# Optimization experiments

Measured on AMD Instinct MI355X. Metric: run time of the kernel, lower is better.

The kernel has to match this reference:

```python
import jax, jax.numpy as jnp
import numpy as np

WINDOW = 512      # sliding window size (causal: keys in [m-WINDOW+1, m])
NEG_INF = -1e30   # large negative instead of -inf for fp16/bf16 safety


def setup_inputs() -> dict:
    key = jax.random.key(0)
    kq, kk, kv = jax.random.split(key, 3)
    B, S, H, Hk, D = 1, 8192, 32, 8, 128
    q = jax.random.normal(kq, (B, S, H, D), dtype=jnp.float32)
    k = jax.random.normal(kk, (B, S, Hk, D), dtype=jnp.float32)
    v = jax.random.normal(kv, (B, S, Hk, D), dtype=jnp.float32)
    return {"q": q, "k": k, "v": v}


def _swa_causal(q, k, v, window):
    """Causal sliding-window attention with GQA, banded (no SxS matrix)."""
    B, S, H, D = q.shape
    Hk = k.shape[2]
    G = H // Hk                      # query heads per kv head
    C = window                        # query block size
    nb = S // C                       # number of query blocks (S divisible by C here)
    L = 2 * window - 1                # kv window width per query block
    pad = window - 1
    scale = 1.0 / jnp.sqrt(jnp.asarray(D, q.dtype))

    # pad keys/values at the front so every block can gather a full window
    kp = jnp.pad(k, ((0, 0), (pad, 0), (0, 0), (0, 0)))
    vp = jnp.pad(v, ((0, 0), (pad, 0), (0, 0), (0, 0)))

    # block queries: [B, nb, C, Hk, G, D]
    qb = q.reshape(B, nb, C, Hk, G, D)

    # kv windows: block n sees padded positions [n*C, n*C + L)
    starts = jnp.arange(nb) * C                      # [nb]
    idx = starts[:, None] + jnp.arange(L)[None, :]   # [nb, L] padded coords
    kw = kp[:, idx]                                  # [B, nb, L, Hk, D]
    vw = vp[:, idx]                                  # [B, nb, L, Hk, D]

    # banded scores: [B, nb, Hk, G, C, L]
    scores = jnp.einsum('bnchgd,bnlhd->bnhgcl', qb, kw) * scale

    # mask: query i (global m = n*C + i), kv slot j (global n_pos = n*C + j - pad)
    # causal window: i <= j <= i + window - 1 ; plus n_pos >= 0
    i = jnp.arange(C)
    j = jnp.arange(L)
    band = (j[None, :] >= i[:, None]) & (j[None, :] <= i[:, None] + window - 1)  # [C, L]
    valid_n = (starts[:, None] + j[None, :] - pad) >= 0                          # [nb, L]
    mask = band[None, :, :] & valid_n[:, None, :]                                # [nb, C, L]

    scores = jnp.where(mask[:, None, None, :, :][None], scores, NEG_INF)
    p = jax.nn.softmax(scores, axis=-1)              # [B, nb, Hk, G, C, L]

    o = jnp.einsum('bnhgcl,bnlhd->bnchgd', p, vw)    # [B, nb, C, Hk, G, D]
    return o.reshape(B, S, H, D)


def reference(q, k, v):
    return _swa_causal(q, k, v, WINDOW)
```

## Files before the change

kernel.cpp:

```cpp
#include <hip/hip_runtime.h>

#define NH   32
#define NHK  8
#define D    128
#define QB   128
#define KB   64
#define NT   128

typedef float f32x16 __attribute__((ext_vector_type(16)));
typedef short bf16x8 __attribute__((ext_vector_type(8)));
typedef unsigned int uint4v __attribute__((ext_vector_type(4)));

__device__ __forceinline__ unsigned cvtpk(float lo, float hi) {
  unsigned r;
  asm("v_cvt_pk_bf16_f32 %0, %1, %2" : "=v"(r) : "v"(lo), "v"(hi));
  return r;
}
__device__ __forceinline__ void gload16(const void* g, void* l) {
  __builtin_amdgcn_global_load_lds(
      (__attribute__((address_space(1))) void*)g,
      (__attribute__((address_space(3))) void*)l, 16, 0, 0);
}

__device__ __forceinline__ int kidx(int j, int col) {
  return (((j >> 1) << 8) + ((j & 1) << 7) + col) ^ (((j >> 1) & 15) << 3);
}
__device__ __forceinline__ int vidx(int d, int j) {
  return (((d >> 1) << 7) + ((d & 1) << 6) + j) ^ (((d >> 1) & 15) << 3);
}

__global__ __launch_bounds__(256)
void prep_kv(const float* __restrict__ kg, const float* __restrict__ vg,
             short* __restrict__ kpre, short* __restrict__ vpre)
{
  int blk = blockIdx.x;
  int tid = threadIdx.x;
  bool isV = blk >= (NHK * NT);
  int lb   = isV ? blk - NHK * NT : blk;
  int hk   = lb >> 7;
  int t    = lb & 127;
  if (!isV) {
    int j  = tid >> 2;
    int dq = (tid & 3) * 32;
    const float* kp = kg + ((size_t)(t*KB + j) * NHK + hk) * D + dq;
    short* dst = kpre + (((size_t)(hk*NT + t)) << 13);
    #pragma unroll
    for (int c = 0; c < 4; ++c) {
      float4 a  = *(const float4*)(kp + c*8);
      float4 b2 = *(const float4*)(kp + c*8 + 4);
      uint4v u;
      u[0] = cvtpk(a.x, a.y);   u[1] = cvtpk(a.z, a.w);
      u[2] = cvtpk(b2.x, b2.y); u[3] = cvtpk(b2.z, b2.w);
      *(uint4v*)&dst[kidx(j, dq + c*8)] = u;
    }
  } else {
    int d0 = (tid & 31) * 4;
    int j0 = (tid >> 5) * 8;
    float tv[8][4];
    #pragma unroll
    for (int r = 0; r < 8; ++r) {
      float4 x = *(const float4*)(vg + ((size_t)(t*KB + j0 + r) * NHK + hk) * D + d0);
      tv[r][0]=x.x; tv[r][1]=x.y; tv[r][2]=x.z; tv[r][3]=x.w;
    }
    short* dst = vpre + (((size_t)(hk*NT + t)) << 13);
    #pragma unroll
    for (int c = 0; c < 4; ++c) {
      int d = d0 + c;
      uint4v u;
      u[0] = cvtpk(tv[0][c], tv[1][c]);
      u[1] = cvtpk(tv[2][c], tv[3][c]);
      u[2] = cvtpk(tv[4][c], tv[5][c]);
      u[3] = cvtpk(tv[6][c], tv[7][c]);
      *(uint4v*)&dst[vidx(d, j0)] = u;
    }
  }
}

__global__ __launch_bounds__(256, 2)
void swa_fwd(const float* __restrict__ qg, const short* __restrict__ kpre,
             const short* __restrict__ vpre, float* __restrict__ og)
{
  __shared__ __align__(16) short lds_k[2][KB * D];
  __shared__ __align__(16) short lds_v[2][KB * D];

  const int tid  = threadIdx.x;
  const int lane = tid & 63;
  const int w    = tid >> 6;
  const int il   = lane & 31;
  const int half = lane >> 5;

  int b    = blockIdx.x;
  int lidx = (b & 7) * 256 + (b >> 3);
  int hk   = lidx >> 8;
  int rem  = lidx & 255;
  int bq   = rem >> 2;
  int h    = hk * 4 + (rem & 3);
  int qs   = bq * QB;

  const float qscale = 0.088388347648318447f * 1.4426950408889634f;

  bf16x8 qf[8];
  {
    const float* qp = qg + ((size_t)(qs + 32*w + il) * NH + h) * D + half * 8;
    #pragma unroll
    for (int ks = 0; ks < 8; ++ks) {
      float4 a = *(const float4*)(qp + ks*16);
      float4 c = *(const float4*)(qp + ks*16 + 4);
      uint4v u;
      u[0] = cvtpk(a.x*qscale, a.y*qscale);
      u[1] = cvtpk(a.z*qscale, a.w*qscale);
      u[2] = cvtpk(c.x*qscale, c.y*qscale);
      u[3] = cvtpk(c.z*qscale, c.w*qscale);
      qf[ks] = __builtin_bit_cast(bf16x8, u);
    }
  }

  f32x16 acc_o[4];
  #pragma unroll
  for (int dt = 0; dt < 4; ++dt)
    #pragma unroll
    for (int r = 0; r < 16; ++r) acc_o[dt][r] = 0.0f;

  float l0 = 0.0f, l1 = 0.0f, l2 = 0.0f, l3 = 0.0f;

  int t_lo = 2*bq - 8; if (t_lo < 0) t_lo = 0;
  int t_hi = 2*bq + 1;
  const int iw_min = qs + 32*w;

  const short* gkb = kpre + (((size_t)hk * NT) << 13);
  const short* gvb = vpre + (((size_t)hk * NT) << 13);
  const int lo = w * 2048;
  const int go = lo + lane * 8;

  asm volatile("s_waitcnt vmcnt(0)" ::: "memory");
  {
    const short* gk = gkb + ((size_t)t_lo << 13);
    const short* gv = gvb + ((size_t)t_lo << 13);
    short* lk = &lds_k[t_lo & 1][0];
    short* lv = &lds_v[t_lo & 1][0];
    #pragma unroll
    for (int i = 0; i < 4; ++i) gload16(gk + go + i*512, lk + lo + i*512);
    #pragma unroll
    for (int i = 0; i < 4; ++i) gload16(gv + go + i*512, lv + lo + i*512);
  }

  for (int t = t_lo; t <= t_hi; ++t) {
    const int kt = t * KB;
    const int bb = t & 1;

    if (t < t_hi) {
      const short* gk = gkb + ((size_t)(t+1) << 13);
      const short* gv = gvb + ((size_t)(t+1) << 13);
      short* lk = &lds_k[bb ^ 1][0];
      short* lv = &lds_v[bb ^ 1][0];
      #pragma unroll
      for (int i = 0; i < 4; ++i) gload16(gk + go + i*512, lk + lo + i*512);
      #pragma unroll
      for (int i = 0; i < 4; ++i) gload16(gv + go + i*512, lv + lo + i*512);
      asm volatile("s_waitcnt vmcnt(8)" ::: "memory");
    } else {
      asm volatile("s_waitcnt vmcnt(0)" ::: "memory");
    }
    __builtin_amdgcn_s_barrier();
    __builtin_amdgcn_sched_barrier(0);

    bool skip = (kt > iw_min + 31) || (kt + KB - 1 < iw_min - 511);
    if (!skip) {
      const short* lk = &lds_k[bb][0];
      const short* lv = &lds_v[bb][0];

      f32x16 acc_s[2];
      #pragma unroll
      for (int mt = 0; mt < 2; ++mt)
        #pragma unroll
        for (int r = 0; r < 16; ++r) acc_s[mt][r] = 0.0f;

      __builtin_amdgcn_s_setprio(1);
      #pragma unroll
      for (int ks = 0; ks < 8; ++ks) {
        #pragma unroll
        for (int mt = 0; mt < 2; ++mt) {
          int jrow = mt*32 + il;
          bf16x8 a = *(const bf16x8*)&lk[kidx(jrow, ks*16 + half*8)];
          acc_s[mt] = __builtin_amdgcn_mfma_f32_32x32x16_bf16(a, qf[ks], acc_s[mt], 0, 0, 0);
        }
      }
      __builtin_amdgcn_s_setprio(0);

      bool do_causal = (kt + KB - 1 > iw_min);
      bool do_window = (kt < iw_min + 31 - 511);
      if (do_causal || do_window) {
        int base0 = kt - iw_min - il + 4*half;
        #pragma unroll
        for (int mt = 0; mt < 2; ++mt)
          #pragma unroll
          for (int r = 0; r < 16; ++r) {
            int delta = base0 + 32*mt + (r & 3) + 8*(r >> 2);
            if ((do_causal && delta > 0) || (do_window && delta < -511))
              acc_s[mt][r] = -1e30f;
          }
      }

      #pragma unroll
      for (int mt = 0; mt < 2; ++mt) {
        float p[16];
        #pragma unroll
        for (int r = 0; r < 16; ++r)
          p[r] = __builtin_amdgcn_exp2f(acc_s[mt][r]);
        l0 += p[0] + p[4];  l1 += p[1] + p[5];
        l2 += p[2] + p[6];  l3 += p[3] + p[7];
        l0 += p[8] + p[12]; l1 += p[9] + p[13];
        l2 += p[10]+ p[14]; l3 += p[11]+ p[15];

        unsigned pkw[8];
        #pragma unroll
        for (int hb = 0; hb < 2; ++hb) {
          int bs = hb * 8;
          unsigned X1 = cvtpk(p[bs+0], p[bs+1]);
          unsigned X2 = cvtpk(p[bs+2], p[bs+3]);
          unsigned Y1 = cvtpk(p[bs+4], p[bs+5]);
          unsigned Y2 = cvtpk(p[bs+6], p[bs+7]);
          asm("v_permlane32_swap_b32 %0, %1" : "+v"(X1), "+v"(Y1));
          asm("v_permlane32_swap_b32 %0, %1" : "+v"(X2), "+v"(Y2));
          pkw[hb*4 + 0] = X1; pkw[hb*4 + 1] = X2;
          pkw[hb*4 + 2] = Y1; pkw[hb*4 + 3] = Y2;
        }
        __builtin_amdgcn_s_setprio(1);
        #pragma unroll
        for (int ksl = 0; ksl < 2; ++ksl) {
          int ks = mt*2 + ksl;
          uint4v pu;
          pu[0] = pkw[ksl*4+0]; pu[1] = pkw[ksl*4+1];
          pu[2] = pkw[ksl*4+2]; pu[3] = pkw[ksl*4+3];
          bf16x8 pb = __builtin_bit_cast(bf16x8, pu);
          #pragma unroll
          for (int dt = 0; dt < 4; ++dt) {
            int d = dt*32 + il;
            bf16x8 a = *(const bf16x8*)&lv[vidx(d, ks*16 + half*8)];
            acc_o[dt] = __builtin_amdgcn_mfma_f32_32x32x16_bf16(a, pb, acc_o[dt], 0, 0, 0);
          }
        }
        __builtin_amdgcn_s_setprio(0);
      }
    }
    __builtin_amdgcn_s_barrier();
  }

  float l_lane = (l0 + l1) + (l2 + l3);
  float l_tot  = l_lane + __shfl_xor(l_lane, 32);
  float inv_l  = 1.0f / l_tot;
  const size_t orow = ((size_t)(qs + 32*w + il) * NH + h) * D;
  #pragma unroll
  for (int dt = 0; dt < 4; ++dt)
    #pragma unroll
    for (int rg = 0; rg < 4; ++rg) {
      float4 o;
      o.x = acc_o[dt][rg*4+0] * inv_l;
      o.y = acc_o[dt][rg*4+1] * inv_l;
      o.z = acc_o[dt][rg*4+2] * inv_l;
      o.w = acc_o[dt][rg*4+3] * inv_l;
      *(float4*)(og + orow + dt*32 + 8*rg + 4*half) = o;
    }
}

__global__ __launch_bounds__(256, 2)
void swa_fwd_fb(const float* __restrict__ qg, const float* __restrict__ kg,
                const float* __restrict__ vg, float* __restrict__ og)
{
  __shared__ __align__(16) short lds_k[KB * D];
  __shared__ __align__(16) short lds_v[D * KB];

  const int tid  = threadIdx.x;
  const int lane = tid & 63;
  const int w    = tid >> 6;
  const int il   = lane & 31;
  const int half = lane >> 5;

  int b    = blockIdx.x;
  int lidx = (b & 7) * 256 + (b >> 3);
  int hk   = lidx >> 8;
  int rem  = lidx & 255;
  int bq   = rem >> 2;
  int h    = hk * 4 + (rem & 3);
  int qs   = bq * 128;

  const float qscale = 0.088388347648318447f * 1.4426950408889634f;

  bf16x8 qf[8];
  {
    const float* qp = qg + ((size_t)(qs + 32*w + il) * NH + h) * D + half * 8;
    #pragma unroll
    for (int ks = 0; ks < 8; ++ks) {
      float4 a = *(const float4*)(qp + ks*16);
      float4 c = *(const float4*)(qp + ks*16 + 4);
      uint4v u;
      u[0] = cvtpk(a.x*qscale, a.y*qscale);
      u[1] = cvtpk(a.z*qscale, a.w*qscale);
      u[2] = cvtpk(c.x*qscale, c.y*qscale);
      u[3] = cvtpk(c.z*qscale, c.w*qscale);
      qf[ks] = __builtin_bit_cast(bf16x8, u);
    }
  }

  f32x16 acc_o[4];
  #pragma unroll
  for (int dt = 0; dt < 4; ++dt)
    #pragma unroll
    for (int r = 0; r < 16; ++r) acc_o[dt][r] = 0.0f;

  float l0 = 0.0f, l1 = 0.0f, l2 = 0.0f, l3 = 0.0f;

  int t_lo = 2*bq - 8; if (t_lo < 0) t_lo = 0;
  int t_hi = 2*bq + 1;
  const int iw_min = qs + 32*w;

  for (int t = t_lo; t <= t_hi; ++t) {
    const int kt = t * KB;
    {
      int j  = tid >> 2;
      int dq = (tid & 3) * 32;
      const float* kp = kg + ((size_t)(kt + j) * NHK + hk) * D + dq;
      #pragma unroll
      for (int c = 0; c < 4; ++c) {
        float4 a  = *(const float4*)(kp + c*8);
        float4 d2 = *(const float4*)(kp + c*8 + 4);
        uint4v u;
        u[0] = cvtpk(a.x, a.y);   u[1] = cvtpk(a.z, a.w);
        u[2] = cvtpk(d2.x, d2.y); u[3] = cvtpk(d2.z, d2.w);
        *(uint4v*)&lds_k[kidx(j, dq + c*8)] = u;
      }
    }
    {
      int d0 = (tid & 31) * 4;
      int j0 = (tid >> 5) * 8;
      float tv[8][4];
      #pragma unroll
      for (int r = 0; r < 8; ++r) {
        float4 x = *(const float4*)(vg + ((size_t)(kt + j0 + r) * NHK + hk) * D + d0);
        tv[r][0]=x.x; tv[r][1]=x.y; tv[r][2]=x.z; tv[r][3]=x.w;
      }
      #pragma unroll
      for (int c = 0; c < 4; ++c) {
        int d = d0 + c;
        uint4v u;
        u[0] = cvtpk(tv[0][c], tv[1][c]);
        u[1] = cvtpk(tv[2][c], tv[3][c]);
        u[2] = cvtpk(tv[4][c], tv[5][c]);
        u[3] = cvtpk(tv[6][c], tv[7][c]);
        *(uint4v*)&lds_v[vidx(d, j0)] = u;
      }
    }
    __syncthreads();

    bool skip = (kt > iw_min + 31) || (kt + KB - 1 < iw_min - 511);
    if (!skip) {
      f32x16 acc_s[2];
      #pragma unroll
      for (int mt = 0; mt < 2; ++mt)
        #pragma unroll
        for (int r = 0; r < 16; ++r) acc_s[mt][r] = 0.0f;

      #pragma unroll
      for (int ks = 0; ks < 8; ++ks) {
        #pragma unroll
        for (int mt = 0; mt < 2; ++mt) {
          int jrow = mt*32 + il;
          bf16x8 a = *(const bf16x8*)&lds_k[kidx(jrow, ks*16 + half*8)];
          acc_s[mt] = __builtin_amdgcn_mfma_f32_32x32x16_bf16(a, qf[ks], acc_s[mt], 0, 0, 0);
        }
      }

      bool do_causal = (kt + KB - 1 > iw_min);
      bool do_window = (kt < iw_min + 31 - 511);
      if (do_causal || do_window) {
        int base0 = kt - iw_min - il + 4*half;
        #pragma unroll
        for (int mt = 0; mt < 2; ++mt)
          #pragma unroll
          for (int r = 0; r < 16; ++r) {
            int delta = base0 + 32*mt + (r & 3) + 8*(r >> 2);
            if ((do_causal && delta > 0) || (do_window && delta < -511))
              acc_s[mt][r] = -1e30f;
          }
      }

      #pragma unroll
      for (int mt = 0; mt < 2; ++mt) {
        float p[16];
        #pragma unroll
        for (int r = 0; r < 16; ++r)
          p[r] = __builtin_amdgcn_exp2f(acc_s[mt][r]);
        l0 += p[0] + p[4];  l1 += p[1] + p[5];
        l2 += p[2] + p[6];  l3 += p[3] + p[7];
        l0 += p[8] + p[12]; l1 += p[9] + p[13];
        l2 += p[10]+ p[14]; l3 += p[11]+ p[15];

        unsigned pkw[8];
        #pragma unroll
        for (int hb = 0; hb < 2; ++hb) {
          int bs = hb * 8;
          unsigned X1 = cvtpk(p[bs+0], p[bs+1]);
          unsigned X2 = cvtpk(p[bs+2], p[bs+3]);
          unsigned Y1 = cvtpk(p[bs+4], p[bs+5]);
          unsigned Y2 = cvtpk(p[bs+6], p[bs+7]);
          asm("v_permlane32_swap_b32 %0, %1" : "+v"(X1), "+v"(Y1));
          asm("v_permlane32_swap_b32 %0, %1" : "+v"(X2), "+v"(Y2));
          pkw[hb*4 + 0] = X1; pkw[hb*4 + 1] = X2;
          pkw[hb*4 + 2] = Y1; pkw[hb*4 + 3] = Y2;
        }
        #pragma unroll
        for (int ksl = 0; ksl < 2; ++ksl) {
          int ks = mt*2 + ksl;
          uint4v pu;
          pu[0] = pkw[ksl*4+0]; pu[1] = pkw[ksl*4+1];
          pu[2] = pkw[ksl*4+2]; pu[3] = pkw[ksl*4+3];
          bf16x8 pb = __builtin_bit_cast(bf16x8, pu);
          #pragma unroll
          for (int dt = 0; dt < 4; ++dt) {
            int d = dt*32 + il;
            bf16x8 a = *(const bf16x8*)&lds_v[vidx(d, ks*16 + half*8)];
            acc_o[dt] = __builtin_amdgcn_mfma_f32_32x32x16_bf16(a, pb, acc_o[dt], 0, 0, 0);
          }
        }
      }
    }
    __syncthreads();
  }

  float l_lane = (l0 + l1) + (l2 + l3);
  float l_tot  = l_lane + __shfl_xor(l_lane, 32);
  float inv_l  = 1.0f / l_tot;
  const size_t orow = ((size_t)(qs + 32*w + il) * NH + h) * D;
  #pragma unroll
  for (int dt = 0; dt < 4; ++dt)
    #pragma unroll
    for (int rg = 0; rg < 4; ++rg) {
      float4 o;
      o.x = acc_o[dt][rg*4+0] * inv_l;
      o.y = acc_o[dt][rg*4+1] * inv_l;
      o.z = acc_o[dt][rg*4+2] * inv_l;
      o.w = acc_o[dt][rg*4+3] * inv_l;
      *(float4*)(og + orow + dt*32 + 8*rg + 4*half) = o;
    }
}

extern "C" void kernel_launch(void* const* d_in, const int* in_sizes, int n_in,
                              void* d_out, int out_size, void* d_ws, size_t ws_size,
                              hipStream_t stream) {
  const float* q = (const float*)d_in[0];
  const float* k = (const float*)d_in[1];
  const float* v = (const float*)d_in[2];
  float* o = (float*)d_out;
  const size_t per = (size_t)NHK * NT * KB * D;
  const size_t need = 2 * per * sizeof(short);
  if (ws_size >= need) {
    short* kpre = (short*)d_ws;
    short* vpre = kpre + per;
    hipLaunchKernelGGL(prep_kv, dim3(2 * NHK * NT), dim3(256), 0, stream, k, v, kpre, vpre);
    hipLaunchKernelGGL(swa_fwd, dim3(2048), dim3(256), 0, stream, q, kpre, vpre, o);
  } else {
    hipLaunchKernelGGL(swa_fwd_fb, dim3(2048), dim3(256), 0, stream, q, k, v, o);
  }
}
```

Before: 146.8 us.

## Halve query block to 64 rows with 2 waves and drop KV double buffering

Shrinks each workgroup to 64 query rows handled by 2 waves, doubling the grid to 4096 blocks. KV tiles are single-buffered and loaded synchronously each iteration (load, wait, barrier), which halves LDS to 32KB per block so more blocks can be resident. The aim is more parallelism and occupancy, with latency hidden by other resident blocks. The cost is no intra-block prefetch overlap and more total KV traffic, since each KV tile is now reloaded by twice as many blocks.

```diff
diff --git a/kernel.cpp b/kernel.cpp
--- a/kernel.cpp
+++ b/kernel.cpp
@@ -3,7 +3,7 @@
 #define NH   32
 #define NHK  8
 #define D    128
-#define QB   128
+#define QB   64
 #define KB   64
 #define NT   128
 
@@ -76,12 +76,12 @@
   }
 }
 
-__global__ __launch_bounds__(256, 2)
+__global__ __launch_bounds__(128, 2)
 void swa_fwd(const float* __restrict__ qg, const short* __restrict__ kpre,
              const short* __restrict__ vpre, float* __restrict__ og)
 {
-  __shared__ __align__(16) short lds_k[2][KB * D];
-  __shared__ __align__(16) short lds_v[2][KB * D];
+  __shared__ __align__(16) short lds_k[KB * D];
+  __shared__ __align__(16) short lds_v[KB * D];
 
   const int tid  = threadIdx.x;
   const int lane = tid & 63;
@@ -90,9 +90,9 @@
   const int half = lane >> 5;
 
   int b    = blockIdx.x;
-  int lidx = (b & 7) * 256 + (b >> 3);
-  int hk   = lidx >> 8;
-  int rem  = lidx & 255;
+  int lidx = (b & 7) * 512 + (b >> 3);
+  int hk   = lidx >> 9;
+  int rem  = lidx & 511;
   int bq   = rem >> 2;
   int h    = hk * 4 + (rem & 3);
   int qs   = bq * QB;
@@ -123,52 +123,32 @@
 
   float l0 = 0.0f, l1 = 0.0f, l2 = 0.0f, l3 = 0.0f;
 
-  int t_lo = 2*bq - 8; if (t_lo < 0) t_lo = 0;
-  int t_hi = 2*bq + 1;
+  int t_lo = bq - 8; if (t_lo < 0) t_lo = 0;
+  int t_hi = bq;
   const int iw_min = qs + 32*w;
 
   const short* gkb = kpre + (((size_t)hk * NT) << 13);
   const short* gvb = vpre + (((size_t)hk * NT) << 13);
-  const int lo = w * 2048;
+  const int lo = w * 4096;
   const int go = lo + lane * 8;
-
-  asm volatile("s_waitcnt vmcnt(0)" ::: "memory");
-  {
-    const short* gk = gkb + ((size_t)t_lo << 13);
-    const short* gv = gvb + ((size_t)t_lo << 13);
-    short* lk = &lds_k[t_lo & 1][0];
-    short* lv = &lds_v[t_lo & 1][0];
-    #pragma unroll
-    for (int i = 0; i < 4; ++i) gload16(gk + go + i*512, lk + lo + i*512);
-    #pragma unroll
-    for (int i = 0; i < 4; ++i) gload16(gv + go + i*512, lv + lo + i*512);
-  }
 
   for (int t = t_lo; t <= t_hi; ++t) {
     const int kt = t * KB;
-    const int bb = t & 1;
-
-    if (t < t_hi) {
-      const short* gk = gkb + ((size_t)(t+1) << 13);
-      const short* gv = gvb + ((size_t)(t+1) << 13);
-      short* lk = &lds_k[bb ^ 1][0];
-      short* lv = &lds_v[bb ^ 1][0];
-      #pragma unroll
-      for (int i = 0; i < 4; ++i) gload16(gk + go + i*512, lk + lo + i*512);
-      #pragma unroll
-      for (int i = 0; i < 4; ++i) gload16(gv + go + i*512, lv + lo + i*512);
-      asm volatile("s_waitcnt vmcnt(8)" ::: "memory");
-    } else {
-      asm volatile("s_waitcnt vmcnt(0)" ::: "memory");
-    }
+
+    {
+      const short* gk = gkb + ((size_t)t << 13);
+      const short* gv = gvb + ((size_t)t << 13);
+      #pragma unroll
+      for (int i = 0; i < 8; ++i) gload16(gk + go + i*512, &lds_k[0] + lo + i*512);
+      #pragma unroll
+      for (int i = 0; i < 8; ++i) gload16(gv + go + i*512, &lds_v[0] + lo + i*512);
+    }
+    asm volatile("s_waitcnt vmcnt(0)" ::: "memory");
     __builtin_amdgcn_s_barrier();
     __builtin_amdgcn_sched_barrier(0);
 
     bool skip = (kt > iw_min + 31) || (kt + KB - 1 < iw_min - 511);
     if (!skip) {
-      const short* lk = &lds_k[bb][0];
-      const short* lv = &lds_v[bb][0];
-
       f32x16 acc_s[2];
       #pragma unroll
       for (int mt = 0; mt < 2; ++mt)
@@ -181,7 +161,7 @@
         #pragma unroll
         for (int mt = 0; mt < 2; ++mt) {
           int jrow = mt*32 + il;
-          bf16x8 a = *(const bf16x8*)&lk[kidx(jrow, ks*16 + half*8)];
+          bf16x8 a = *(const bf16x8*)&lds_k[kidx(jrow, ks*16 + half*8)];
           acc_s[mt] = __builtin_amdgcn_mfma_f32_32x32x16_bf16(a, qf[ks], acc_s[mt], 0, 0, 0);
         }
       }
@@ -236,14 +216,14 @@
           #pragma unroll
           for (int dt = 0; dt < 4; ++dt) {
             int d = dt*32 + il;
-            bf16x8 a = *(const bf16x8*)&lv[vidx(d, ks*16 + half*8)];
+            bf16x8 a = *(const bf16x8*)&lds_v[vidx(d, ks*16 + half*8)];
             acc_o[dt] = __builtin_amdgcn_mfma_f32_32x32x16_bf16(a, pb, acc_o[dt], 0, 0, 0);
           }
         }
         __builtin_amdgcn_s_setprio(0);
       }
     }
-    __builtin_amdgcn_s_barrier();
+    if (t < t_hi) __builtin_amdgcn_s_barrier();
   }
 
   float l_lane = (l0 + l1) + (l2 + l3);
@@ -457,7 +437,7 @@
     short* kpre = (short*)d_ws;
     short* vpre = kpre + per;
     hipLaunchKernelGGL(prep_kv, dim3(2 * NHK * NT), dim3(256), 0, stream, k, v, kpre, vpre);
-    hipLaunchKernelGGL(swa_fwd, dim3(2048), dim3(256), 0, stream, q, kpre, vpre, o);
+    hipLaunchKernelGGL(swa_fwd, dim3(4096), dim3(128), 0, stream, q, kpre, vpre, o);
   } else {
     hipLaunchKernelGGL(swa_fwd_fb, dim3(2048), dim3(256), 0, stream, q, k, v, o);
   }
```

Result: no change. 146.9 us (+0.1%).

## Load two KV tiles per synchronous stage instead of double-buffered prefetch

Applied to the files above, without the earlier changes.

Replaces the double-buffered prefetch loop, which loaded the next 64-key tile while computing the current one, with a loop that loads two consecutive tiles (128 keys) into both LDS buffers at once. It then waits for the loads and processes both tiles before the next load. This halves the number of barriers and load phases per block. In exchange, global-to-LDS loads no longer overlap with MFMA compute within a workgroup, so latency hiding now depends on other resident workgroups.

```diff
diff --git a/kernel.cpp b/kernel.cpp
--- a/kernel.cpp
+++ b/kernel.cpp
@@ -124,126 +124,113 @@
   float l0 = 0.0f, l1 = 0.0f, l2 = 0.0f, l3 = 0.0f;
 
   int t_lo = 2*bq - 8; if (t_lo < 0) t_lo = 0;
-  int t_hi = 2*bq + 1;
+  const int T_lo = t_lo >> 1;
+  const int T_hi = bq;
   const int iw_min = qs + 32*w;
 
   const short* gkb = kpre + (((size_t)hk * NT) << 13);
   const short* gvb = vpre + (((size_t)hk * NT) << 13);
-  const int lo = w * 2048;
-  const int go = lo + lane * 8;
-
-  asm volatile("s_waitcnt vmcnt(0)" ::: "memory");
-  {
-    const short* gk = gkb + ((size_t)t_lo << 13);
-    const short* gv = gvb + ((size_t)t_lo << 13);
-    short* lk = &lds_k[t_lo & 1][0];
-    short* lv = &lds_v[t_lo & 1][0];
-    #pragma unroll
-    for (int i = 0; i < 4; ++i) gload16(gk + go + i*512, lk + lo + i*512);
-    #pragma unroll
-    for (int i = 0; i < 4; ++i) gload16(gv + go + i*512, lv + lo + i*512);
-  }
-
-  for (int t = t_lo; t <= t_hi; ++t) {
-    const int kt = t * KB;
-    const int bb = t & 1;
-
-    if (t < t_hi) {
-      const short* gk = gkb + ((size_t)(t+1) << 13);
-      const short* gv = gvb + ((size_t)(t+1) << 13);
-      short* lk = &lds_k[bb ^ 1][0];
-      short* lv = &lds_v[bb ^ 1][0];
-      #pragma unroll
-      for (int i = 0; i < 4; ++i) gload16(gk + go + i*512, lk + lo + i*512);
-      #pragma unroll
-      for (int i = 0; i < 4; ++i) gload16(gv + go + i*512, lv + lo + i*512);
-      asm volatile("s_waitcnt vmcnt(8)" ::: "memory");
-    } else {
-      asm volatile("s_waitcnt vmcnt(0)" ::: "memory");
-    }
+  const int lo2 = w * 4096;
+  const int go2 = lo2 + lane * 8;
+
+  for (int T = T_lo; T <= T_hi; ++T) {
+    {
+      const short* gk = gkb + ((size_t)T << 14);
+      const short* gv = gvb + ((size_t)T << 14);
+      #pragma unroll
+      for (int i = 0; i < 8; ++i) gload16(gk + go2 + i*512, &lds_k[0][0] + lo2 + i*512);
+      #pragma unroll
+      for (int i = 0; i < 8; ++i) gload16(gv + go2 + i*512, &lds_v[0][0] + lo2 + i*512);
+    }
+    asm volatile("s_waitcnt vmcnt(0)" ::: "memory");
     __builtin_amdgcn_s_barrier();
     __builtin_amdgcn_sched_barrier(0);
 
-    bool skip = (kt > iw_min + 31) || (kt + KB - 1 < iw_min - 511);
-    if (!skip) {
-      const short* lk = &lds_k[bb][0];
-      const short* lv = &lds_v[bb][0];
-
-      f32x16 acc_s[2];
-      #pragma unroll
-      for (int mt = 0; mt < 2; ++mt)
-        #pragma unroll
-        for (int r = 0; r < 16; ++r) acc_s[mt][r] = 0.0f;
-
-      __builtin_amdgcn_s_setprio(1);
-      #pragma unroll
-      for (int ks = 0; ks < 8; ++ks) {
+    #pragma unroll
+    for (int st = 0; st < 2; ++st) {
+      const int t  = 2*T + st;
+      const int kt = t * KB;
+      const short* lk = &lds_k[st][0];
+      const short* lv = &lds_v[st][0];
+
+      bool skip = (kt > iw_min + 31) || (kt + KB - 1 < iw_min - 511);
+      if (!skip) {
+        f32x16 acc_s[2];
+        #pragma unroll
+        for (int mt = 0; mt < 2; ++mt)
+          #pragma unroll
+          for (int r = 0; r < 16; ++r) acc_s[mt][r] = 0.0f;
+
+        __builtin_amdgcn_s_setprio(1);
+        #pragma unroll
+        for (int ks = 0; ks < 8; ++ks) {
+          #pragma unroll
+          for (int mt = 0; mt < 2; ++mt) {
+            int jrow = mt*32 + il;
+            bf16x8 a = *(const bf16x8*)&lk[kidx(jrow, ks*16 + half*8)];
+            acc_s[mt] = __builtin_amdgcn_mfma_f32_32x32x16_bf16(a, qf[ks], acc_s[mt], 0, 0, 0);
+          }
+        }
+        __builtin_amdgcn_s_setprio(0);
+
+        bool do_causal = (kt + KB - 1 > iw_min);
+        bool do_window = (kt < iw_min + 31 - 511);
+        if (do_causal || do_window) {
+          int base0 = kt - iw_min - il + 4*half;
+          #pragma unroll
+          for (int mt = 0; mt < 2; ++mt)
+            #pragma unroll
+            for (int r = 0; r < 16; ++r) {
+              int delta = base0 + 32*mt + (r & 3) + 8*(r >> 2);
+              if ((do_causal && delta > 0) || (do_window && delta < -511))
+                acc_s[mt][r] = -1e30f;
+            }
+        }
+
         #pragma unroll
         for (int mt = 0; mt < 2; ++mt) {
-          int jrow = mt*32 + il;
-          bf16x8 a = *(const bf16x8*)&lk[kidx(jrow, ks*16 + half*8)];
-          acc_s[mt] = __builtin_amdgcn_mfma_f32_32x32x16_bf16(a, qf[ks], acc_s[mt], 0, 0, 0);
-        }
-      }
-      __builtin_amdgcn_s_setprio(0);
-
-      bool do_causal = (kt + KB - 1 > iw_min);
-      bool do_window = (kt < iw_min + 31 - 511);
-      if (do_causal || do_window) {
-        int base0 = kt - iw_min - il + 4*half;
-        #pragma unroll
-        for (int mt = 0; mt < 2; ++mt)
-          #pragma unroll
-          for (int r = 0; r < 16; ++r) {
-            int delta = base0 + 32*mt + (r & 3) + 8*(r >> 2);
-            if ((do_causal && delta > 0) || (do_window && delta < -511))
-              acc_s[mt][r] = -1e30f;
+          float p[16];
+          #pragma unroll
+          for (int r = 0; r < 16; ++r)
+            p[r] = __builtin_amdgcn_exp2f(acc_s[mt][r]);
+          l0 += p[0] + p[4];  l1 += p[1] + p[5];
+          l2 += p[2] + p[6];  l3 += p[3] + p[7];
+          l0 += p[8] + p[12]; l1 += p[9] + p[13];
+          l2 += p[10]+ p[14]; l3 += p[11]+ p[15];
+
+          unsigned pkw[8];
+          #pragma unroll
+          for (int hb = 0; hb < 2; ++hb) {
+            int bs = hb * 8;
+            unsigned X1 = cvtpk(p[bs+0], p[bs+1]);
+            unsigned X2 = cvtpk(p[bs+2], p[bs+3]);
+            unsigned Y1 = cvtpk(p[bs+4], p[bs+5]);
+            unsigned Y2 = cvtpk(p[bs+6], p[bs+7]);
+            asm("v_permlane32_swap_b32 %0, %1" : "+v"(X1), "+v"(Y1));
+            asm("v_permlane32_swap_b32 %0, %1" : "+v"(X2), "+v"(Y2));
+            pkw[hb*4 + 0] = X1; pkw[hb*4 + 1] = X2;
+            pkw[hb*4 + 2] = Y1; pkw[hb*4 + 3] = Y2;
           }
-      }
-
-      #pragma unroll
-      for (int mt = 0; mt < 2; ++mt) {
-        float p[16];
-        #pragma unroll
-        for (int r = 0; r < 16; ++r)
-          p[r] = __builtin_amdgcn_exp2f(acc_s[mt][r]);
-        l0 += p[0] + p[4];  l1 += p[1] + p[5];
-        l2 += p[2] + p[6];  l3 += p[3] + p[7];
-        l0 += p[8] + p[12]; l1 += p[9] + p[13];
-        l2 += p[10]+ p[14]; l3 += p[11]+ p[15];
-
-        unsigned pkw[8];
-        #pragma unroll
-        for (int hb = 0; hb < 2; ++hb) {
-          int bs = hb * 8;
-          unsigned X1 = cvtpk(p[bs+0], p[bs+1]);
-          unsigned X2 = cvtpk(p[bs+2], p[bs+3]);
-          unsigned Y1 = cvtpk(p[bs+4], p[bs+5]);
-          unsigned Y2 = cvtpk(p[bs+6], p[bs+7]);
-          asm("v_permlane32_swap_b32 %0, %1" : "+v"(X1), "+v"(Y1));
-          asm("v_permlane32_swap_b32 %0, %1" : "+v"(X2), "+v"(Y2));
-          pkw[hb*4 + 0] = X1; pkw[hb*4 + 1] = X2;
-          pkw[hb*4 + 2] = Y1; pkw[hb*4 + 3] = Y2;
-        }
-        __builtin_amdgcn_s_setprio(1);
-        #pragma unroll
-        for (int ksl = 0; ksl < 2; ++ksl) {
-          int ks = mt*2 + ksl;
-          uint4v pu;
-          pu[0] = pkw[ksl*4+0]; pu[1] = pkw[ksl*4+1];
-          pu[2] = pkw[ksl*4+2]; pu[3] = pkw[ksl*4+3];
-          bf16x8 pb = __builtin_bit_cast(bf16x8, pu);
-          #pragma unroll
-          for (int dt = 0; dt < 4; ++dt) {
-            int d = dt*32 + il;
-            bf16x8 a = *(const bf16x8*)&lv[vidx(d, ks*16 + half*8)];
-            acc_o[dt] = __builtin_amdgcn_mfma_f32_32x32x16_bf16(a, pb, acc_o[dt], 0, 0, 0);
+          __builtin_amdgcn_s_setprio(1);
+          #pragma unroll
+          for (int ksl = 0; ksl < 2; ++ksl) {
+            int ks = mt*2 + ksl;
+            uint4v pu;
+            pu[0] = pkw[ksl*4+0]; pu[1] = pkw[ksl*4+1];
+            pu[2] = pkw[ksl*4+2]; pu[3] = pkw[ksl*4+3];
+            bf16x8 pb = __builtin_bit_cast(bf16x8, pu);
+            #pragma unroll
+            for (int dt = 0; dt < 4; ++dt) {
+              int d = dt*32 + il;
+              bf16x8 a = *(const bf16x8*)&lv[vidx(d, ks*16 + half*8)];
+              acc_o[dt] = __builtin_amdgcn_mfma_f32_32x32x16_bf16(a, pb, acc_o[dt], 0, 0, 0);
+            }
           }
-        }
-        __builtin_amdgcn_s_setprio(0);
-      }
-    }
-    __builtin_amdgcn_s_barrier();
+          __builtin_amdgcn_s_setprio(0);
+        }
+      }
+    }
+    if (T < T_hi) __builtin_amdgcn_s_barrier();
   }
 
   float l_lane = (l0 + l1) + (l2 + l3);
```

Measured after the change: 135.8 us (median of 2 runs). 7.5% less time.
